# Kernel optimization log

Measured on AMD Instinct MI355X. Metric: run time of the kernel, lower is better.

Reference implementation:

```python
import jax, jax.numpy as jnp
import numpy as np

N = 50000
E = 800000
IN = 128
H = 4
C = 32  # hidden_channels per head; H*C == 128 so every layer is 128->128
NEG_SLOPE = 0.2  # PyG GATConv default negative_slope


def setup_inputs() -> dict:
    key = jax.random.key(0)
    ks = jax.random.split(key, 20)
    inp = {
        "x": jax.random.normal(ks[0], (N, IN), dtype=jnp.float32),
        "edge_index": jax.random.randint(ks[1], (2, E), 0, N, dtype=jnp.int64),
    }
    # 4 GATConv layers, each 128 -> (H=4, C=32), concat -> 128
    for i in range(4):
        k = jax.random.split(ks[2 + i], 4)
        inp[f"W{i+1}"] = jax.random.normal(k[0], (IN, H * C), dtype=jnp.float32) * 0.08
        inp[f"as{i+1}"] = jax.random.normal(k[1], (H, C), dtype=jnp.float32) * 0.08
        inp[f"ad{i+1}"] = jax.random.normal(k[2], (H, C), dtype=jnp.float32) * 0.08
        inp[f"b{i+1}"] = jnp.zeros((H * C,), dtype=jnp.float32)
    return inp


def gat_conv(x, src, dst, W, a_src, a_dst, bias):
    n = x.shape[0]
    h = (x @ W).reshape(n, H, C)                       # [N,H,C]
    alpha_src = jnp.einsum("nhc,hc->nh", h, a_src)      # [N,H]
    alpha_dst = jnp.einsum("nhc,hc->nh", h, a_dst)      # [N,H]
    e = jax.nn.leaky_relu(alpha_src[src] + alpha_dst[dst], NEG_SLOPE)  # [E,H]
    # segment softmax over incoming edges of each dst node
    emax = jax.ops.segment_max(e, dst, num_segments=n)
    emax = jnp.where(jnp.isfinite(emax), emax, 0.0)
    ex = jnp.exp(e - emax[dst])
    denom = jax.ops.segment_sum(ex, dst, num_segments=n)
    alpha = ex / denom[dst]                             # [E,H]
    msg = h[src] * alpha[:, :, None]                    # [E,H,C]
    out = jax.ops.segment_sum(msg, dst, num_segments=n) # [N,H,C]
    return out.reshape(n, H * C) + bias


def reference(x, edge_index, W1, as1, ad1, b1, W2, as2, ad2, b2,
              W3, as3, ad3, b3, W4, as4, ad4, b4):
    # PyG GATConv add_self_loops=True: append self-loops once
    loops = jnp.arange(N, dtype=edge_index.dtype)
    src = jnp.concatenate([edge_index[0], loops])
    dst = jnp.concatenate([edge_index[1], loops])
    x1 = jax.nn.relu(gat_conv(x, src, dst, W1, as1, ad1, b1))
    x2 = jax.nn.relu(gat_conv(x1, src, dst, W2, as2, ad2, b2))
    x3 = jax.nn.relu(gat_conv(x2, src, dst, W3, as3, ad3, b3))
    x4 = gat_conv(x3, src, dst, W4, as4, ad4, b4)
    return x4
```

## Files before the change

kernel.cpp:

```cpp
#include <hip/hip_runtime.h>
#include <hip/hip_fp16.h>
#include <math.h>

#define NNODES 50000
#define NEDGES 800000
#define NTOT   (NNODES + NEDGES)
#define GROWS  96
#define DEGCAP 64
#define NBLK1  ((NEDGES + 2047) / 2048)
#define NBUCK  98
#define SUBCAP 64

typedef _Float16 half8 __attribute__((ext_vector_type(8)));
typedef _Float16 half4 __attribute__((ext_vector_type(4)));
typedef float    f32x4 __attribute__((ext_vector_type(4)));


__global__ __launch_bounds__(512) void bin1_kernel(const int* __restrict__ ei,
                                                   unsigned int* __restrict__ region,
                                                   int* __restrict__ cnt) {
  __shared__ int lcnt[NBUCK];
  int t = threadIdx.x, blk = blockIdx.x;
  for (int i = t; i < NBUCK; i += 512) lcnt[i] = 0;
  __syncthreads();
  int e0 = blk * 2048;
  #pragma unroll
  for (int q = 0; q < 4; ++q) {
    int e = e0 + q * 512 + t;
    if (e < NEDGES) {
      int src = ei[e];
      int dst = ei[NEDGES + e];
      int b = dst >> 9;
      int r = atomicAdd(&lcnt[b], 1);
      if (r < SUBCAP)
        region[((size_t)blk * NBUCK + b) * SUBCAP + r] =
            (unsigned int)src | ((unsigned int)(dst & 511) << 20);
    }
  }
  __syncthreads();
  for (int i = t; i < NBUCK; i += 512) cnt[blk * NBUCK + i] = min(lcnt[i], SUBCAP);
}


__global__ __launch_bounds__(1024) void bin2_kernel(const unsigned int* __restrict__ region,
                                                    const int* __restrict__ cnt,
                                                    int* __restrict__ counts,
                                                    unsigned short* __restrict__ adj) {
  __shared__ int cur[512];
  int t = threadIdx.x, b = blockIdx.x;
  int nodeBase = b << 9;
  if (t < 512) {
    cur[t] = 1;
    int node = nodeBase + t;
    if (node < NNODES) adj[(size_t)node * DEGCAP] = (unsigned short)node;
  }
  __syncthreads();
  int wave = t >> 6, lane = t & 63;
  for (int i = wave; i < NBLK1; i += 16) {
    int ci = cnt[i * NBUCK + b];
    const unsigned int* sub = region + ((size_t)i * NBUCK + b) * SUBCAP;
    for (int j = lane; j < ci; j += 64) {
      unsigned int u = sub[j];
      int dl  = (int)(u >> 20);
      int src = (int)(u & 0xFFFFF);
      int slot = atomicAdd(&cur[dl], 1);
      if (slot < DEGCAP)
        adj[(size_t)(nodeBase + dl) * DEGCAP + slot] = (unsigned short)src;
    }
  }
  __syncthreads();
  if (t < 512 && nodeBase + t < NNODES) counts[nodeBase + t] = cur[t];
}


__global__ __launch_bounds__(256) void wprep4_kernel(
    const float* __restrict__ W0, const float* __restrict__ W1,
    const float* __restrict__ W2, const float* __restrict__ W3,
    _Float16* __restrict__ hi, _Float16* __restrict__ lo) {
  int id = blockIdx.x * 256 + threadIdx.x;
  int l = id >> 14, o = id & 16383;
  const float* W = (l == 0) ? W0 : (l == 1) ? W1 : (l == 2) ? W2 : W3;
  int n = o >> 7, k = o & 127;
  float v = W[k * 128 + n];
  _Float16 h = (_Float16)v;
  hi[id] = h;
  lo[id] = (_Float16)(v - (float)h);
}


__global__ __launch_bounds__(384) void gemm_mfma_kernel(
    const float* __restrict__ X, const _Float16* __restrict__ Wthi,
    const _Float16* __restrict__ Wtlo,
    const float* __restrict__ a_src, const float* __restrict__ a_dst,
    _Float16* __restrict__ Hh, float* __restrict__ alps, float* __restrict__ alpd) {
  __shared__ _Float16 whi[128 * 136];
  __shared__ _Float16 wlo[128 * 136];
  int t = threadIdx.x;

  for (int i = t; i < 2048; i += 384) {
    int n = i >> 4, koff = (i & 15) * 8;
    *(half8*)&whi[n * 136 + koff] = *(const half8*)&Wthi[n * 128 + koff];
    *(half8*)&wlo[n * 136 + koff] = *(const half8*)&Wtlo[n * 128 + koff];
  }
  __syncthreads();

  int wave = t >> 6, lane = t & 63;
  int row  = blockIdx.x * GROWS + wave * 16 + (lane & 15);
  int kg   = (lane >> 4) * 8;
  bool valid = row < NNODES;

  f32x4 acc[8];
  #pragma unroll
  for (int tl = 0; tl < 8; ++tl) acc[tl] = (f32x4){0.f, 0.f, 0.f, 0.f};

  #pragma unroll
  for (int kt = 0; kt < 4; ++kt) {
    int k0 = kt * 32 + kg;
    half8 bh, bl;
    if (valid) {
      const float* xp = X + (size_t)row * 128 + k0;
      float4 f0 = *(const float4*)xp;
      float4 f1 = *(const float4*)(xp + 4);
      float fv[8] = {f0.x, f0.y, f0.z, f0.w, f1.x, f1.y, f1.z, f1.w};
      #pragma unroll
      for (int j = 0; j < 8; ++j) {
        _Float16 h = (_Float16)fv[j];
        bh[j] = h;
        bl[j] = (_Float16)(fv[j] - (float)h);
      }
    } else {
      #pragma unroll
      for (int j = 0; j < 8; ++j) { bh[j] = (_Float16)0.f; bl[j] = (_Float16)0.f; }
    }
    #pragma unroll
    for (int tl = 0; tl < 8; ++tl) {
      int aoff = (tl * 16 + (lane & 15)) * 136 + k0;
      half8 ah = *(const half8*)&whi[aoff];
      half8 al = *(const half8*)&wlo[aoff];
      acc[tl] = __builtin_amdgcn_mfma_f32_16x16x32_f16(ah, bh, acc[tl], 0, 0, 0);
      acc[tl] = __builtin_amdgcn_mfma_f32_16x16x32_f16(ah, bl, acc[tl], 0, 0, 0);
      acc[tl] = __builtin_amdgcn_mfma_f32_16x16x32_f16(al, bh, acc[tl], 0, 0, 0);
    }
  }

  int cg = (lane >> 4) * 4;
  float ps[4] = {0.f, 0.f, 0.f, 0.f}, pd[4] = {0.f, 0.f, 0.f, 0.f};
  #pragma unroll
  for (int tl = 0; tl < 8; ++tl) {
    int col0 = tl * 16 + cg;
    float4 as4 = *(const float4*)&a_src[col0];
    float4 ad4 = *(const float4*)&a_dst[col0];
    int hd = tl >> 1;
    ps[hd] += acc[tl][0] * as4.x + acc[tl][1] * as4.y + acc[tl][2] * as4.z + acc[tl][3] * as4.w;
    pd[hd] += acc[tl][0] * ad4.x + acc[tl][1] * ad4.y + acc[tl][2] * ad4.z + acc[tl][3] * ad4.w;
    if (valid) {
      half4 hv;
      hv[0] = (_Float16)acc[tl][0]; hv[1] = (_Float16)acc[tl][1];
      hv[2] = (_Float16)acc[tl][2]; hv[3] = (_Float16)acc[tl][3];
      *(half4*)&Hh[(size_t)row * 128 + col0] = hv;
    }
  }
  #pragma unroll
  for (int hd = 0; hd < 4; ++hd) {
    ps[hd] += __shfl_xor(ps[hd], 16, 64);
    ps[hd] += __shfl_xor(ps[hd], 32, 64);
    pd[hd] += __shfl_xor(pd[hd], 16, 64);
    pd[hd] += __shfl_xor(pd[hd], 32, 64);
  }
  if (valid && lane < 16) {
    *(f32x4*)&alps[row * 4] = (f32x4){ps[0], ps[1], ps[2], ps[3]};
    *(f32x4*)&alpd[row * 4] = (f32x4){pd[0], pd[1], pd[2], pd[3]};
  }
}


#define AGG_BODY(JB)                                                    \
  {                                                                     \
    int jj = (JB) + e4;                                                 \
    int sj = s_lds[wslot][jj];                                          \
    float pj = p_lds[wslot][jj * 4 + hd_b];                             \
    const half8 hv = *(const half8*)(&Hh[(size_t)sj * 128 + col0]);     \
    a0 = fmaf(pj, (float)hv[0], a0);                                    \
    a1 = fmaf(pj, (float)hv[1], a1);                                    \
    a2 = fmaf(pj, (float)hv[2], a2);                                    \
    a3 = fmaf(pj, (float)hv[3], a3);                                    \
    a4 = fmaf(pj, (float)hv[4], a4);                                    \
    a5 = fmaf(pj, (float)hv[5], a5);                                    \
    a6 = fmaf(pj, (float)hv[6], a6);                                    \
    a7 = fmaf(pj, (float)hv[7], a7);                                    \
  }

__global__ __launch_bounds__(256) void agg_kernel(
    const _Float16* __restrict__ Hh, const float* __restrict__ alps,
    const float* __restrict__ alpd, const int* __restrict__ counts,
    const unsigned short* __restrict__ adj, const float* __restrict__ bias,
    float* __restrict__ out, int relu_flag) {
  __shared__ float p_lds[4][68 * 4];
  __shared__ int   s_lds[4][68];
  int wslot = threadIdx.x >> 6;
  int wid = (blockIdx.x * 256 + threadIdx.x) >> 6;
  if (wid >= NNODES) return;
  int lane = threadIdx.x & 63;
  int e4   = lane >> 4;
  int cidx = lane & 15;
  int hd_b = cidx >> 2;
  int col0 = cidx * 8;
  int nc = min(counts[wid], DEGCAP);

  float4 adv = *(const float4*)(&alpd[wid * 4]);

  float p0 = 0.f, p1 = 0.f, p2 = 0.f, p3 = 0.f;
  int src = 0;
  if (lane < nc) {
    src = (int)adj[(size_t)wid * DEGCAP + lane];
    float4 av = *(const float4*)(&alps[src * 4]);
    float v0 = av.x + adv.x, v1 = av.y + adv.y;
    float v2 = av.z + adv.z, v3 = av.w + adv.w;
    float e0 = (v0 > 0.f) ? v0 : 0.2f * v0;
    float e1 = (v1 > 0.f) ? v1 : 0.2f * v1;
    float e2v = (v2 > 0.f) ? v2 : 0.2f * v2;
    float e3 = (v3 > 0.f) ? v3 : 0.2f * v3;
    p0 = __expf(fminf(e0, 60.f));
    p1 = __expf(fminf(e1, 60.f));
    p2 = __expf(fminf(e2v, 60.f));
    p3 = __expf(fminf(e3, 60.f));
  }
  s_lds[wslot][lane] = src;
  *(float4*)(&p_lds[wslot][lane * 4]) = make_float4(p0, p1, p2, p3);
  if (lane < 4) {
    s_lds[wslot][64 + lane] = 0;
    *(float4*)(&p_lds[wslot][(64 + lane) * 4]) = make_float4(0.f, 0.f, 0.f, 0.f);
  }
  float q0 = p0, q1 = p1, q2 = p2, q3 = p3;
  #pragma unroll
  for (int off = 1; off < 64; off <<= 1) {
    q0 += __shfl_xor(q0, off, 64);
    q1 += __shfl_xor(q1, off, 64);
    q2 += __shfl_xor(q2, off, 64);
    q3 += __shfl_xor(q3, off, 64);
  }
  asm volatile("s_waitcnt lgkmcnt(0)" ::: "memory");

  float a0 = 0.f, a1 = 0.f, a2 = 0.f, a3 = 0.f;
  float a4 = 0.f, a5 = 0.f, a6 = 0.f, a7 = 0.f;
  int j = 0;
  for (; j + 16 <= nc; j += 16) {
    AGG_BODY(j) AGG_BODY(j + 4) AGG_BODY(j + 8) AGG_BODY(j + 12)
  }
  if (j + 8 <= nc) {
    AGG_BODY(j) AGG_BODY(j + 4)
    j += 8;
  }
  if (j < nc) {
    AGG_BODY(j) AGG_BODY(j + 4)
  }

  #pragma unroll
  for (int off = 16; off < 64; off <<= 1) {
    a0 += __shfl_xor(a0, off, 64);
    a1 += __shfl_xor(a1, off, 64);
    a2 += __shfl_xor(a2, off, 64);
    a3 += __shfl_xor(a3, off, 64);
    a4 += __shfl_xor(a4, off, 64);
    a5 += __shfl_xor(a5, off, 64);
    a6 += __shfl_xor(a6, off, 64);
    a7 += __shfl_xor(a7, off, 64);
  }

  if (lane < 16) {
    float sh = (hd_b == 0) ? q0 : (hd_b == 1) ? q1 : (hd_b == 2) ? q2 : q3;
    float inv = 1.0f / sh;
    float4 bv0 = *(const float4*)(&bias[col0]);
    float4 bv1 = *(const float4*)(&bias[col0 + 4]);
    float o0 = a0 * inv + bv0.x, o1 = a1 * inv + bv0.y;
    float o2 = a2 * inv + bv0.z, o3 = a3 * inv + bv0.w;
    float o4 = a4 * inv + bv1.x, o5 = a5 * inv + bv1.y;
    float o6 = a6 * inv + bv1.z, o7 = a7 * inv + bv1.w;
    if (relu_flag) {
      o0 = fmaxf(o0, 0.f); o1 = fmaxf(o1, 0.f); o2 = fmaxf(o2, 0.f); o3 = fmaxf(o3, 0.f);
      o4 = fmaxf(o4, 0.f); o5 = fmaxf(o5, 0.f); o6 = fmaxf(o6, 0.f); o7 = fmaxf(o7, 0.f);
    }
    *(float4*)(&out[(size_t)wid * 128 + col0])     = make_float4(o0, o1, o2, o3);
    *(float4*)(&out[(size_t)wid * 128 + col0 + 4]) = make_float4(o4, o5, o6, o7);
  }
}


extern "C" void kernel_launch(void* const* d_in, const int* in_sizes, int n_in,
                              void* d_out, int out_size, void* d_ws, size_t ws_size,
                              hipStream_t stream) {
  const float* x  = (const float*)d_in[0];
  const int*   ei = (const int*)d_in[1];
  const float* W[4]  = {(const float*)d_in[2],  (const float*)d_in[6],
                        (const float*)d_in[10], (const float*)d_in[14]};
  const float* As[4] = {(const float*)d_in[3],  (const float*)d_in[7],
                        (const float*)d_in[11], (const float*)d_in[15]};
  const float* Ad[4] = {(const float*)d_in[4],  (const float*)d_in[8],
                        (const float*)d_in[12], (const float*)d_in[16]};
  const float* Bs[4] = {(const float*)d_in[5],  (const float*)d_in[9],
                        (const float*)d_in[13], (const float*)d_in[17]};

  char* p = (char*)d_ws;
  auto alloc = [&](size_t bytes) {
    char* r = p;
    p += (bytes + 255) & ~(size_t)255;
    return r;
  };
  unsigned int*   region = (unsigned int*)alloc(sizeof(unsigned int) * (size_t)NBLK1 * NBUCK * SUBCAP);
  int*            cnt    = (int*)alloc(sizeof(int) * NBLK1 * NBUCK);
  int*            counts = (int*)alloc(sizeof(int) * NNODES);
  unsigned short* adj    = (unsigned short*)alloc(sizeof(unsigned short) * (size_t)NNODES * DEGCAP);
  float*          alps   = (float*)alloc(sizeof(float) * NNODES * 4);
  float*          alpd   = (float*)alloc(sizeof(float) * NNODES * 4);
  float*          bufA   = (float*)alloc(sizeof(float) * (size_t)NNODES * 128);
  _Float16*       Hh     = (_Float16*)alloc(sizeof(_Float16) * (size_t)NNODES * 128);
  _Float16*       Wthi   = (_Float16*)alloc(sizeof(_Float16) * 4 * 128 * 128);
  _Float16*       Wtlo   = (_Float16*)alloc(sizeof(_Float16) * 4 * 128 * 128);

  bin1_kernel  <<<NBLK1, 512, 0, stream>>>(ei, region, cnt);
  bin2_kernel  <<<NBUCK, 1024, 0, stream>>>(region, cnt, counts, adj);
  wprep4_kernel<<<256, 256, 0, stream>>>(W[0], W[1], W[2], W[3], Wthi, Wtlo);

  const float* cur = x;
  for (int l = 0; l < 4; ++l) {
    gemm_mfma_kernel<<<(NNODES + GROWS - 1) / GROWS, 384, 0, stream>>>(
        cur, Wthi + l * 16384, Wtlo + l * 16384, As[l], Ad[l], Hh, alps, alpd);
    float* o = (l == 3) ? (float*)d_out : bufA;
    agg_kernel<<<(NNODES * 64 + 255) / 256, 256, 0, stream>>>(
        Hh, alps, alpd, counts, adj, Bs[l], o, (l < 3) ? 1 : 0);
    cur = o;
  }
}
```

Baseline: 281.4 us.

## Process two row tiles per wave in GEMM and enlarge edge binning blocks

The GEMM kernel now has each wave compute two 16-row tiles, so every W fragment loaded from LDS feeds six MFMAs instead of three. Rows per block double to 192, which halves the number of blocks and the per-block staging of W into LDS. The binning kernel also handles 4096 edges per block with a larger per-bucket sub-capacity of 96, so fewer blocks and partial regions are needed. In exchange, register use goes up from doubling the accumulators, and the bin buffers become larger.

```diff
diff --git a/kernel.cpp b/kernel.cpp
--- a/kernel.cpp
+++ b/kernel.cpp
@@ -5,11 +5,12 @@
 #define NNODES 50000
 #define NEDGES 800000
 #define NTOT   (NNODES + NEDGES)
-#define GROWS  96
+#define GROWS  192
 #define DEGCAP 64
-#define NBLK1  ((NEDGES + 2047) / 2048)
+#define EPB    4096
+#define NBLK1  ((NEDGES + EPB - 1) / EPB)
 #define NBUCK  98
-#define SUBCAP 64
+#define SUBCAP 96
 
 typedef _Float16 half8 __attribute__((ext_vector_type(8)));
 typedef _Float16 half4 __attribute__((ext_vector_type(4)));
@@ -23,9 +24,9 @@
   int t = threadIdx.x, blk = blockIdx.x;
   for (int i = t; i < NBUCK; i += 512) lcnt[i] = 0;
   __syncthreads();
-  int e0 = blk * 2048;
-  #pragma unroll
-  for (int q = 0; q < 4; ++q) {
+  int e0 = blk * EPB;
+  #pragma unroll
+  for (int q = 0; q < EPB / 512; ++q) {
     int e = e0 + q * 512 + t;
     if (e < NEDGES) {
       int src = ei[e];
@@ -105,71 +106,99 @@
   __syncthreads();
 
   int wave = t >> 6, lane = t & 63;
-  int row  = blockIdx.x * GROWS + wave * 16 + (lane & 15);
-  int kg   = (lane >> 4) * 8;
-  bool valid = row < NNODES;
-
-  f32x4 acc[8];
-  #pragma unroll
-  for (int tl = 0; tl < 8; ++tl) acc[tl] = (f32x4){0.f, 0.f, 0.f, 0.f};
+  int r0 = blockIdx.x * GROWS + wave * 32 + (lane & 15);
+  int r1 = r0 + 16;
+  int kg = (lane >> 4) * 8;
+  bool v0 = r0 < NNODES, v1 = r1 < NNODES;
+
+  f32x4 acc0[8], acc1[8];
+  #pragma unroll
+  for (int tl = 0; tl < 8; ++tl) {
+    acc0[tl] = (f32x4){0.f, 0.f, 0.f, 0.f};
+    acc1[tl] = (f32x4){0.f, 0.f, 0.f, 0.f};
+  }
 
   #pragma unroll
   for (int kt = 0; kt < 4; ++kt) {
     int k0 = kt * 32 + kg;
-    half8 bh, bl;
-    if (valid) {
-      const float* xp = X + (size_t)row * 128 + k0;
+    half8 bh0, bl0, bh1, bl1;
+    if (v0) {
+      const float* xp = X + (size_t)r0 * 128 + k0;
       float4 f0 = *(const float4*)xp;
       float4 f1 = *(const float4*)(xp + 4);
       float fv[8] = {f0.x, f0.y, f0.z, f0.w, f1.x, f1.y, f1.z, f1.w};
       #pragma unroll
       for (int j = 0; j < 8; ++j) {
         _Float16 h = (_Float16)fv[j];
-        bh[j] = h;
-        bl[j] = (_Float16)(fv[j] - (float)h);
+        bh0[j] = h;
+        bl0[j] = (_Float16)(fv[j] - (float)h);
       }
     } else {
       #pragma unroll
-      for (int j = 0; j < 8; ++j) { bh[j] = (_Float16)0.f; bl[j] = (_Float16)0.f; }
+      for (int j = 0; j < 8; ++j) { bh0[j] = (_Float16)0.f; bl0[j] = (_Float16)0.f; }
+    }
+    if (v1) {
+      const float* xp = X + (size_t)r1 * 128 + k0;
+      float4 f0 = *(const float4*)xp;
+      float4 f1 = *(const float4*)(xp + 4);
+      float fv[8] = {f0.x, f0.y, f0.z, f0.w, f1.x, f1.y, f1.z, f1.w};
+      #pragma unroll
+      for (int j = 0; j < 8; ++j) {
+        _Float16 h = (_Float16)fv[j];
+        bh1[j] = h;
+        bl1[j] = (_Float16)(fv[j] - (float)h);
+      }
+    } else {
+      #pragma unroll
+      for (int j = 0; j < 8; ++j) { bh1[j] = (_Float16)0.f; bl1[j] = (_Float16)0.f; }
     }
     #pragma unroll
     for (int tl = 0; tl < 8; ++tl) {
       int aoff = (tl * 16 + (lane & 15)) * 136 + k0;
       half8 ah = *(const half8*)&whi[aoff];
       half8 al = *(const half8*)&wlo[aoff];
-      acc[tl] = __builtin_amdgcn_mfma_f32_16x16x32_f16(ah, bh, acc[tl], 0, 0, 0);
-      acc[tl] = __builtin_amdgcn_mfma_f32_16x16x32_f16(ah, bl, acc[tl], 0, 0, 0);
-      acc[tl] = __builtin_amdgcn_mfma_f32_16x16x32_f16(al, bh, acc[tl], 0, 0, 0);
+      acc0[tl] = __builtin_amdgcn_mfma_f32_16x16x32_f16(ah, bh0, acc0[tl], 0, 0, 0);
+      acc0[tl] = __builtin_amdgcn_mfma_f32_16x16x32_f16(ah, bl0, acc0[tl], 0, 0, 0);
+      acc0[tl] = __builtin_amdgcn_mfma_f32_16x16x32_f16(al, bh0, acc0[tl], 0, 0, 0);
+      acc1[tl] = __builtin_amdgcn_mfma_f32_16x16x32_f16(ah, bh1, acc1[tl], 0, 0, 0);
+      acc1[tl] = __builtin_amdgcn_mfma_f32_16x16x32_f16(ah, bl1, acc1[tl], 0, 0, 0);
+      acc1[tl] = __builtin_amdgcn_mfma_f32_16x16x32_f16(al, bh1, acc1[tl], 0, 0, 0);
     }
   }
 
   int cg = (lane >> 4) * 4;
-  float ps[4] = {0.f, 0.f, 0.f, 0.f}, pd[4] = {0.f, 0.f, 0.f, 0.f};
-  #pragma unroll
-  for (int tl = 0; tl < 8; ++tl) {
-    int col0 = tl * 16 + cg;
-    float4 as4 = *(const float4*)&a_src[col0];
-    float4 ad4 = *(const float4*)&a_dst[col0];
-    int hd = tl >> 1;
-    ps[hd] += acc[tl][0] * as4.x + acc[tl][1] * as4.y + acc[tl][2] * as4.z + acc[tl][3] * as4.w;
-    pd[hd] += acc[tl][0] * ad4.x + acc[tl][1] * ad4.y + acc[tl][2] * ad4.z + acc[tl][3] * ad4.w;
-    if (valid) {
-      half4 hv;
-      hv[0] = (_Float16)acc[tl][0]; hv[1] = (_Float16)acc[tl][1];
-      hv[2] = (_Float16)acc[tl][2]; hv[3] = (_Float16)acc[tl][3];
-      *(half4*)&Hh[(size_t)row * 128 + col0] = hv;
-    }
-  }
-  #pragma unroll
-  for (int hd = 0; hd < 4; ++hd) {
-    ps[hd] += __shfl_xor(ps[hd], 16, 64);
-    ps[hd] += __shfl_xor(ps[hd], 32, 64);
-    pd[hd] += __shfl_xor(pd[hd], 16, 64);
-    pd[hd] += __shfl_xor(pd[hd], 32, 64);
-  }
-  if (valid && lane < 16) {
-    *(f32x4*)&alps[row * 4] = (f32x4){ps[0], ps[1], ps[2], ps[3]};
-    *(f32x4*)&alpd[row * 4] = (f32x4){pd[0], pd[1], pd[2], pd[3]};
+  #pragma unroll
+  for (int g = 0; g < 2; ++g) {
+    int row = (g == 0) ? r0 : r1;
+    bool valid = (g == 0) ? v0 : v1;
+    f32x4* acc = (g == 0) ? acc0 : acc1;
+    float ps[4] = {0.f, 0.f, 0.f, 0.f}, pd[4] = {0.f, 0.f, 0.f, 0.f};
+    #pragma unroll
+    for (int tl = 0; tl < 8; ++tl) {
+      int col0 = tl * 16 + cg;
+      float4 as4 = *(const float4*)&a_src[col0];
+      float4 ad4 = *(const float4*)&a_dst[col0];
+      int hd = tl >> 1;
+      ps[hd] += acc[tl][0] * as4.x + acc[tl][1] * as4.y + acc[tl][2] * as4.z + acc[tl][3] * as4.w;
+      pd[hd] += acc[tl][0] * ad4.x + acc[tl][1] * ad4.y + acc[tl][2] * ad4.z + acc[tl][3] * ad4.w;
+      if (valid) {
+        half4 hv;
+        hv[0] = (_Float16)acc[tl][0]; hv[1] = (_Float16)acc[tl][1];
+        hv[2] = (_Float16)acc[tl][2]; hv[3] = (_Float16)acc[tl][3];
+        *(half4*)&Hh[(size_t)row * 128 + col0] = hv;
+      }
+    }
+    #pragma unroll
+    for (int hd = 0; hd < 4; ++hd) {
+      ps[hd] += __shfl_xor(ps[hd], 16, 64);
+      ps[hd] += __shfl_xor(ps[hd], 32, 64);
+      pd[hd] += __shfl_xor(pd[hd], 16, 64);
+      pd[hd] += __shfl_xor(pd[hd], 32, 64);
+    }
+    if (valid && lane < 16) {
+      *(f32x4*)&alps[row * 4] = (f32x4){ps[0], ps[1], ps[2], ps[3]};
+      *(f32x4*)&alpd[row * 4] = (f32x4){pd[0], pd[1], pd[2], pd[3]};
+    }
   }
 }
 
```

Result: no change. 283.2 us (+0.7%).
